# Kernel optimization log

Measured on AMD Instinct MI355X. Metric: run time of the kernel, lower is better.

## Reference

```python
import jax, jax.numpy as jnp
import numpy as np

IN_SHAPE = 4096
H_S = 250        # sender_hidden
H_R = 100        # receiver_hidden
MAX_LEN = 30     # message_shape[0]
VOCAB = 40       # message_shape[1]; EOS = VOCAB-1
OUT_CLS = 512 ** 2  # out_shape[1] ** out_shape[0]


def lstm_cell(x, h, c, W_ih, W_hh, b_ih, b_hh):
    # PyTorch LSTM cell: gate order i, f, g, o
    gates = W_ih @ x + b_ih + W_hh @ h + b_hh
    i, f, g, o = jnp.split(gates, 4)
    c_new = jax.nn.sigmoid(f) * c + jax.nn.sigmoid(i) * jnp.tanh(g)
    h_new = jax.nn.sigmoid(o) * jnp.tanh(c_new)
    return h_new, c_new


def setup_inputs() -> dict:
    key = jax.random.key(0)
    ks = jax.random.split(key, 16)
    s = 0.05
    return {
        "x": jax.random.normal(ks[0], (IN_SHAPE,), dtype=jnp.float32),
        "gumbel_noise": jax.random.gumbel(ks[1], (MAX_LEN, VOCAB), dtype=jnp.float32),
        "W_s1": jax.random.normal(ks[2], (H_S, IN_SHAPE)) * s,
        "b_s1": jnp.zeros((H_S,), jnp.float32),
        "W_ih1": jax.random.normal(ks[3], (4 * H_S, VOCAB)) * s,
        "W_hh1": jax.random.normal(ks[4], (4 * H_S, H_S)) * s,
        "b_ih1": jnp.zeros((4 * H_S,), jnp.float32),
        "b_hh1": jnp.zeros((4 * H_S,), jnp.float32),
        "W_p": jax.random.normal(ks[5], (VOCAB, H_S)) * s,
        "b_p": jnp.zeros((VOCAB,), jnp.float32),
        "W_ih2": jax.random.normal(ks[6], (4 * H_R, VOCAB)) * s,
        "W_hh2": jax.random.normal(ks[7], (4 * H_R, H_R)) * s,
        "b_ih2": jnp.zeros((4 * H_R,), jnp.float32),
        "b_hh2": jnp.zeros((4 * H_R,), jnp.float32),
        "W_r": jax.random.normal(ks[8], (OUT_CLS, H_R)) * s,
        "b_r": jnp.zeros((OUT_CLS,), jnp.float32),
    }


def reference(x, gumbel_noise, W_s1, b_s1, W_ih1, W_hh1, b_ih1, b_hh1,
              W_p, b_p, W_ih2, W_hh2, b_ih2, b_hh2, W_r, b_r):
    dt = x.dtype
    eos = jax.nn.one_hot(VOCAB - 1, VOCAB, dtype=dt)
    # sender: h0 = relu(sender1(x)), c0 = 0, first input = sos = zeros
    h0 = jax.nn.relu(W_s1 @ x + b_s1)
    c0 = jnp.zeros((H_S,), dt)
    sos = jnp.zeros((VOCAB,), dt)
    is_last = jnp.arange(MAX_LEN) == MAX_LEN - 1

    def sender_step(carry, inp):
        h, c, sym, done = carry
        g, last = inp
        nh, nc = lstm_cell(sym, h, c, W_ih1, W_hh1, b_ih1, b_hh1)
        logits = W_p @ nh + b_p
        soft = jax.nn.softmax(logits + g)  # gumbel_softmax, tau=1
        idx = jnp.argmax(soft)
        hard = jax.nn.one_hot(idx, VOCAB, dtype=dt)
        st = hard + soft - jax.lax.stop_gradient(soft)  # straight-through
        # at max length the original appends the plain EOS constant
        emit = jnp.where(last & ~done, eos, st)
        emit = jnp.where(done, eos, emit)
        valid = ~done  # this symbol is part of the message
        new_done = done | (idx == VOCAB - 1) | last
        h = jnp.where(done, h, nh)
        c = jnp.where(done, c, nc)
        sym = jnp.where(done, sym, emit)
        return (h, c, sym, new_done), (emit, valid)

    _, (msg, valid) = jax.lax.scan(
        sender_step, (h0, c0, sos, jnp.array(False)), (gumbel_noise, is_last))

    # receiver LSTM: consume message up to and including first EOS (freeze after)
    def recv_step(carry, inp):
        h, c = carry
        sym, v = inp
        nh, nc = lstm_cell(sym, h, c, W_ih2, W_hh2, b_ih2, b_hh2)
        return (jnp.where(v, nh, h), jnp.where(v, nc, c)), None

    (hR, _), _ = jax.lax.scan(
        recv_step, (jnp.zeros((H_R,), dt), jnp.zeros((H_R,), dt)), (msg, valid))
    return jax.nn.softmax(W_r @ hR + b_r)  # [OUT_CLS]
```

## Files before the change

### kernel.cpp

```cpp
#include <hip/hip_runtime.h>
#include <math.h>

#define HS    250
#define HRr   100
#define VOC   40
#define TMAX  30
#define NCLS  262144
#define KS    10
#define RPB   25

typedef unsigned long long ull;

#define PKNH(wsp, par) ((ull*)(wsp) + (size_t)(par) * 256)
#define PKLP(wsp, par) ((ull*)(wsp) + 512 + (size_t)(par) * 400)
#define PKMSG(wsp)     ((ull*)(wsp) + 1312)
#define WS_SUMS 5024
#define WS_HR   5088
#define WS_ZERO_BYTES 20352

#define TG(wv) ((unsigned)((wv) >> 32))

__device__ __forceinline__ float sigf(float x) { return 1.f / (1.f + expf(-x)); }
__device__ __forceinline__ float lanebc(float v, int l) {
  return __int_as_float(__builtin_amdgcn_readlane(__float_as_int(v), l));
}
__device__ __forceinline__ ull packtv(unsigned tag, float v) {
  return ((ull)tag << 32) | (ull)__float_as_uint(v);
}
__device__ __forceinline__ float lowf(ull w) { return __uint_as_float((unsigned)w); }

__device__ __forceinline__ void st_llc(ull* p, ull v) {
  asm volatile("global_store_dwordx2 %0, %1, off sc0 sc1"
               :: "v"(p), "v"(v) : "memory");
}
__device__ __forceinline__ ull ld_llc(const ull* p) {
  ull r;
  asm volatile("global_load_dwordx2 %0, %1, off sc0 sc1\n\t"
               "s_waitcnt vmcnt(0)"
               : "=v"(r) : "v"(p) : "memory");
  return r;
}

#define SENDER_GATES(P, HV)                                   \
  {                                                           \
    _Pragma("unroll")                                         \
    for (int i = 0; i < 64; i += 4) {                         \
      a0 += whh[i    ] * lanebc(HV, i    );                   \
      a1 += whh[i + 1] * lanebc(HV, i + 1);                   \
      a2 += whh[i + 2] * lanebc(HV, i + 2);                   \
      a3 += whh[i + 3] * lanebc(HV, i + 3);                   \
    }                                                         \
    _Pragma("unroll")                                         \
    for (int i = 0; i < 10; i += 2) {                         \
      a0 += wih[i    ] * lanebc(sv, (P) * 10 + i    );        \
      a1 += wih[i + 1] * lanebc(sv, (P) * 10 + i + 1);        \
    }                                                         \
  }

#define RED(x) ((part[(x)] + part[100 + (x)]) + (part[200 + (x)] + part[300 + (x)]))

__global__ __launch_bounds__(512, 2) void k_sender(
    const float* __restrict__ x,
    const float* __restrict__ W_s1,  const float* __restrict__ b_s1,
    const float* __restrict__ gum,
    const float* __restrict__ W_ih1, const float* __restrict__ W_hh1,
    const float* __restrict__ b_ih1, const float* __restrict__ b_hh1,
    const float* __restrict__ W_p,   const float* __restrict__ b_p,
    const float* __restrict__ W_ih2, const float* __restrict__ W_hh2,
    const float* __restrict__ b_ih2, const float* __restrict__ b_hh2,
    float* __restrict__ ws) {
  __shared__ float part[400];
  __shared__ float h0L[32];
  __shared__ float hx[256];
  __shared__ float lpx[400];
  __shared__ float symx[VOC];
  __shared__ int   doneL;
  __shared__ float gL[400];
  __shared__ float hL[HRr];

  const int b    = blockIdx.x;
  const int t0   = threadIdx.x;
  const int lane = t0 & 63;
  const int w    = t0 >> 6;

  if (b < KS) {
    const int p    = w & 3;
    const int lr   = ((w >> 2) << 6) + lane;
    const bool gact = (lr < 100);
    const int gi   = lr / 25, rr = lr % 25;
    const int grow = gi * 250 + b * RPB + rr;

    float whh[64], wih[10], bsum = 0.f;
    if (gact) {
      #pragma unroll
      for (int i = 0; i < 64; i++) {
        int k = p * 64 + i;
        whh[i] = (k < HS) ? W_hh1[(size_t)grow * HS + k] : 0.f;
      }
      #pragma unroll
      for (int i = 0; i < 10; i++) wih[i] = W_ih1[grow * VOC + p * 10 + i];
      bsum = b_ih1[grow] + b_hh1[grow];
    }
    float wps[RPB];
    if (w == 0) {
      #pragma unroll
      for (int r = 0; r < RPB; r++)
        wps[r] = (lane < VOC) ? W_p[lane * HS + b * RPB + r] : 0.f;
    }
    const float bpv = (lane < VOC) ? b_p[lane] : 0.f;

    {
      const int nr = (w == 7) ? 4 : 3;
      for (int j = 0; j < nr; ++j) {
        const int r = 3 * w + j;
        const float4* wr = (const float4*)(W_s1 + (size_t)(b * RPB + r) * 4096);
        const float4* xr = (const float4*)x;
        float a0 = 0.f, a1 = 0.f, a2 = 0.f, a3 = 0.f;
        #pragma unroll
        for (int q = 0; q < 16; ++q) {
          float4 w4 = wr[lane + (q << 6)], x4 = xr[lane + (q << 6)];
          a0 += w4.x * x4.x; a1 += w4.y * x4.y; a2 += w4.z * x4.z; a3 += w4.w * x4.w;
        }
        float acc = (a0 + a1) + (a2 + a3);
        #pragma unroll
        for (int o = 32; o; o >>= 1) acc += __shfl_down(acc, o);
        if (lane == 0) h0L[r] = acc + b_s1[b * RPB + r];
      }
    }
    __syncthreads();
    if (w == 0 && lane < RPB) {
      float hn0 = fmaxf(h0L[lane], 0.f);
      st_llc(&PKNH(ws, 1)[b * RPB + lane], packtv(1u, hn0));
    }

    float c  = 0.f;
    float sv = 0.f;
    const bool h3v = (192 + lane) < HS;
    const bool l6v = lane < (400 - 384);

    for (int s = 0; s <= TMAX; ++s) {
      float gv = 0.f;
      if (s > 0 && lane < VOC) gv = gum[(s - 1) * VOC + lane];

      if (w == 0) {
        const unsigned need = (unsigned)(s + 1);
        const int par = (s + 1) & 1;
        const ull* nhp = PKNH(ws, par);
        const ull* lpp = PKLP(ws, par);
        const bool lpact = (s > 0);
        const ull* pn0 = nhp + lane;        const ull* pn1 = nhp + 64 + lane;
        const ull* pn2 = nhp + 128 + lane;  const ull* pn3 = nhp + 192 + lane;
        const ull* pl0 = lpp + lane;        const ull* pl1 = lpp + 64 + lane;
        const ull* pl2 = lpp + 128 + lane;  const ull* pl3 = lpp + 192 + lane;
        const ull* pl4 = lpp + 256 + lane;  const ull* pl5 = lpp + 320 + lane;
        const ull* pl6 = lpp + 384 + lane;
        ull hw0, hw1, hw2, hw3, lw0, lw1, lw2, lw3, lw4, lw5, lw6;
        for (;;) {
          asm volatile(
            "global_load_dwordx2 %0, %11, off sc0 sc1\n\t"
            "global_load_dwordx2 %1, %12, off sc0 sc1\n\t"
            "global_load_dwordx2 %2, %13, off sc0 sc1\n\t"
            "global_load_dwordx2 %3, %14, off sc0 sc1\n\t"
            "global_load_dwordx2 %4, %15, off sc0 sc1\n\t"
            "global_load_dwordx2 %5, %16, off sc0 sc1\n\t"
            "global_load_dwordx2 %6, %17, off sc0 sc1\n\t"
            "global_load_dwordx2 %7, %18, off sc0 sc1\n\t"
            "global_load_dwordx2 %8, %19, off sc0 sc1\n\t"
            "global_load_dwordx2 %9, %20, off sc0 sc1\n\t"
            "global_load_dwordx2 %10, %21, off sc0 sc1\n\t"
            "s_waitcnt vmcnt(0)"
            : "=&v"(hw0), "=&v"(hw1), "=&v"(hw2), "=&v"(hw3),
              "=&v"(lw0), "=&v"(lw1), "=&v"(lw2), "=&v"(lw3),
              "=&v"(lw4), "=&v"(lw5), "=&v"(lw6)
            : "v"(pn0), "v"(pn1), "v"(pn2), "v"(pn3),
              "v"(pl0), "v"(pl1), "v"(pl2), "v"(pl3),
              "v"(pl4), "v"(pl5), "v"(pl6)
            : "memory");
          bool ok = TG(hw0) == need && TG(hw1) == need && TG(hw2) == need &&
                    (!h3v || TG(hw3) == need);
          if (lpact) {
            ok = ok && TG(lw0) == need && TG(lw1) == need && TG(lw2) == need &&
                       TG(lw3) == need && TG(lw4) == need && TG(lw5) == need &&
                       (!l6v || TG(lw6) == need);
          }
          if (__all(ok)) break;
        }
        hx[lane] = lowf(hw0); hx[64 + lane] = lowf(hw1); hx[128 + lane] = lowf(hw2);
        if (h3v) hx[192 + lane] = lowf(hw3);
        if (lpact) {
          lpx[lane] = lowf(lw0);        lpx[64 + lane] = lowf(lw1);
          lpx[128 + lane] = lowf(lw2);  lpx[192 + lane] = lowf(lw3);
          lpx[256 + lane] = lowf(lw4);  lpx[320 + lane] = lowf(lw5);
          if (l6v) lpx[384 + lane] = lowf(lw6);
        }
      }
      __syncthreads();

      float hv0 = hx[lane], hv1 = hx[64 + lane], hv2 = hx[128 + lane];
      float hv3 = h3v ? hx[192 + lane] : 0.f;

      if (s > 0) {
        float lg = -INFINITY;
        if (lane < VOC) {
          float acc = bpv + gv;
          #pragma unroll
          for (int m = 0; m < KS; ++m) acc += lpx[m * VOC + lane];
          lg = acc;
        }
        float v = lg; int bi = lane;
        #pragma unroll
        for (int o = 32; o; o >>= 1) {
          float ov = __shfl_down(v, o);
          int   oi = __shfl_down(bi, o);
          if (ov > v) { v = ov; bi = oi; }
        }
        float m  = __shfl(v, 0);
        int  idx = __shfl(bi, 0);
        float e = (lane < VOC) ? expf(lg - m) : 0.f;
        float ssum = e;
        #pragma unroll
        for (int o = 32; o; o >>= 1) ssum += __shfl_down(ssum, o);
        ssum = __shfl(ssum, 0);
        float soft = e / ssum;
        float hard = (lane == idx) ? 1.f : 0.f;
        float st   = (hard + soft) - soft;
        const bool last = (s - 1 == TMAX - 1);
        float emit = last ? ((lane == VOC - 1) ? 1.f : 0.f) : st;
        const bool done = (idx == VOC - 1) || last;
        if (b == 0 && w == 0 && lane < VOC)
          st_llc(&PKMSG(ws)[(s - 1) * VOC + lane],
                 packtv((unsigned)s | (done ? 0x10000u : 0u), emit));
        sv = (lane < VOC) ? emit : 0.f;
        if (done) break;
      }

      if (gact) {
        float a0 = bsum, a1 = 0.f, a2 = 0.f, a3 = 0.f;
        if      (p == 0) SENDER_GATES(0, hv0)
        else if (p == 1) SENDER_GATES(1, hv1)
        else if (p == 2) SENDER_GATES(2, hv2)
        else             SENDER_GATES(3, hv3)
        part[p * 100 + lr] = (a0 + a1) + (a2 + a3);
      }
      __syncthreads();

      if (w == 0) {
        float gi_ = RED(lane < RPB ? lane : 0);
        float gf_ = RED(25 + (lane < RPB ? lane : 0));
        float gg_ = RED(50 + (lane < RPB ? lane : 0));
        float go_ = RED(75 + (lane < RPB ? lane : 0));
        float ig = sigf(gi_), fg = sigf(gf_), gg = tanhf(gg_), og = sigf(go_);
        float cn = fg * c + ig * gg; c = cn;
        float hn = og * tanhf(cn);
        float lpsum = 0.f;
        #pragma unroll
        for (int r = 0; r < RPB; ++r) lpsum += wps[r] * lanebc(hn, r);
        const unsigned nt = (unsigned)(s + 2);
        const int np = (s + 2) & 1;
        if (lane < RPB) st_llc(&PKNH(ws, np)[b * RPB + lane], packtv(nt, hn));
        if (lane < VOC) st_llc(&PKLP(ws, np)[b * VOC + lane], packtv(nt, lpsum));
      }
    }
  } else {
    const bool act = (t0 < 400);
    float wih2[VOC], whh2[HRr], bsum2 = 0.f;
    if (act) {
      #pragma unroll
      for (int i = 0; i < VOC; i++) wih2[i] = W_ih2[t0 * VOC + i];
      #pragma unroll
      for (int i = 0; i < HRr; i++) whh2[i] = W_hh2[t0 * HRr + i];
      bsum2 = b_ih2[t0] + b_hh2[t0];
    }
    float c2 = 0.f, rv0 = 0.f, rv1 = 0.f;

    for (int t = 0; t < TMAX; ++t) {
      if (w == 0) {
        const bool mv = (lane < VOC);
        ull mw = 0;
        for (;;) {
          if (mv) mw = ld_llc(&PKMSG(ws)[t * VOC + lane]);
          bool ok = !mv || ((unsigned)(mw >> 32) & 0xFFFFu) == (unsigned)(t + 1);
          if (__all(ok)) break;
        }
        if (mv) symx[lane] = lowf(mw);
        if (lane == 0) doneL = (int)(((unsigned)(mw >> 32)) >> 16);
      }
      __syncthreads();
      const bool done = (doneL != 0);
      float sv2 = (lane < VOC) ? symx[lane] : 0.f;
      if (act) {
        float a0 = bsum2, a1 = 0.f, a2 = 0.f, a3 = 0.f;
        #pragma unroll
        for (int i = 0; i < VOC; i += 4) {
          a0 += wih2[i    ] * lanebc(sv2, i    );
          a1 += wih2[i + 1] * lanebc(sv2, i + 1);
          a2 += wih2[i + 2] * lanebc(sv2, i + 2);
          a3 += wih2[i + 3] * lanebc(sv2, i + 3);
        }
        #pragma unroll
        for (int i = 0; i < 64; i += 4) {
          a0 += whh2[i    ] * lanebc(rv0, i    );
          a1 += whh2[i + 1] * lanebc(rv0, i + 1);
          a2 += whh2[i + 2] * lanebc(rv0, i + 2);
          a3 += whh2[i + 3] * lanebc(rv0, i + 3);
        }
        #pragma unroll
        for (int i = 0; i < 36; i += 4) {
          a0 += whh2[64 + i    ] * lanebc(rv1, i    );
          a1 += whh2[64 + i + 1] * lanebc(rv1, i + 1);
          a2 += whh2[64 + i + 2] * lanebc(rv1, i + 2);
          a3 += whh2[64 + i + 3] * lanebc(rv1, i + 3);
        }
        gL[t0] = (a0 + a1) + (a2 + a3);
      }
      __syncthreads();
      if (t0 < HRr) {
        float ig = sigf(gL[t0]);
        float fg = sigf(gL[100 + t0]);
        float gg = tanhf(gL[200 + t0]);
        float og = sigf(gL[300 + t0]);
        float cn = fg * c2 + ig * gg; c2 = cn;
        hL[t0] = og * tanhf(cn);
      }
      __syncthreads();
      rv0 = hL[lane];
      rv1 = (lane < 36) ? hL[64 + lane] : 0.f;
      if (done) break;
    }
    if (t0 < HRr) ws[WS_HR + t0] = hL[t0];
  }
}

__global__ __launch_bounds__(256) void k_out(
    const float* __restrict__ W_r, const float* __restrict__ b_r,
    float* __restrict__ ws, float* __restrict__ out) {
  __shared__ float4 h4[25];
  __shared__ float  red[4];
  const int t0 = threadIdx.x;
  if (t0 < 25) h4[t0] = ((const float4*)(ws + WS_HR))[t0];
  __syncthreads();
  const int lane = t0 & 63;
  const int wv   = t0 >> 6;
  const int sl   = lane & 31;
  const int hf   = lane >> 5;
  const int base = blockIdx.x * 128 + wv * 32;
  float accs = 0.f;
  #pragma unroll 4
  for (int i = 0; i < 16; ++i) {
    const int row = base + 2 * i + hf;
    float v = 0.f;
    if (sl < 25) {
      float4 w4 = ((const float4*)W_r)[(size_t)row * 25 + sl];
      float4 hq = h4[sl];
      v = w4.x * hq.x + w4.y * hq.y + w4.z * hq.z + w4.w * hq.w;
    }
    #pragma unroll
    for (int o = 16; o; o >>= 1) v += __shfl_down(v, o, 32);
    float e = 0.f;
    if (sl == 0) { e = expf(v + b_r[row]); accs += e; }
    float eB = __shfl(e, 32);
    if (lane == 0) ((float2*)out)[(base + 2 * i) >> 1] = make_float2(e, eB);
  }
  accs += __shfl_down(accs, 32);
  if (lane == 0) red[wv] = accs;
  __syncthreads();
  if (t0 == 0)
    atomicAdd(&ws[WS_SUMS + (blockIdx.x & 63)], (red[0] + red[1]) + (red[2] + red[3]));
}

__global__ __launch_bounds__(256) void k_scale(const float* __restrict__ ws,
                                               float* __restrict__ out) {
  float s = ws[WS_SUMS + (threadIdx.x & 63)];
  #pragma unroll
  for (int o = 1; o < 64; o <<= 1) s += __shfl_xor(s, o);
  const float rinv = 1.f / s;
  const int i = blockIdx.x * 256 + threadIdx.x;
  float4 e = ((const float4*)out)[i];
  e.x *= rinv; e.y *= rinv; e.z *= rinv; e.w *= rinv;
  ((float4*)out)[i] = e;
}

extern "C" void kernel_launch(void* const* d_in, const int* in_sizes, int n_in,
                              void* d_out, int out_size, void* d_ws, size_t ws_size,
                              hipStream_t stream) {
  const float* x     = (const float*)d_in[0];
  const float* gum   = (const float*)d_in[1];
  const float* W_s1  = (const float*)d_in[2];
  const float* b_s1  = (const float*)d_in[3];
  const float* W_ih1 = (const float*)d_in[4];
  const float* W_hh1 = (const float*)d_in[5];
  const float* b_ih1 = (const float*)d_in[6];
  const float* b_hh1 = (const float*)d_in[7];
  const float* W_p   = (const float*)d_in[8];
  const float* b_p   = (const float*)d_in[9];
  const float* W_ih2 = (const float*)d_in[10];
  const float* W_hh2 = (const float*)d_in[11];
  const float* b_ih2 = (const float*)d_in[12];
  const float* b_hh2 = (const float*)d_in[13];
  const float* W_r   = (const float*)d_in[14];
  const float* b_r   = (const float*)d_in[15];
  float* ws  = (float*)d_ws;
  float* out = (float*)d_out;

  (void)hipMemsetAsync(d_ws, 0, WS_ZERO_BYTES, stream);
  k_sender<<<KS + 1,   512, 0, stream>>>(x, W_s1, b_s1, gum, W_ih1, W_hh1,
                                         b_ih1, b_hh1, W_p, b_p,
                                         W_ih2, W_hh2, b_ih2, b_hh2, ws);
  k_out   <<<NCLS/128, 256, 0, stream>>>(W_r, b_r, ws, out);
  k_scale <<<NCLS/1024,256, 0, stream>>>(ws, out);
}
```

Baseline: 304.3 us.

## Compute sender logits locally from full hidden state instead of exchanging partial sums

Each sender block now computes all 40 logits redundantly from the full gathered hidden vector using W_p rows held in registers (5 rows per wave) with wave reductions. This removes the per-step publication and polling of 400 tagged partial-logit words through the coherent cache, shrinking the cross-block exchange to just the hidden state. It adds redundant compute, an extra block barrier per step and more registers, and the launch bound is relaxed to one block per SM to allow that register growth.

```diff
diff --git a/kernel.cpp b/kernel.cpp
--- a/kernel.cpp
+++ b/kernel.cpp
@@ -12,7 +12,6 @@
 typedef unsigned long long ull;
 
 #define PKNH(wsp, par) ((ull*)(wsp) + (size_t)(par) * 256)
-#define PKLP(wsp, par) ((ull*)(wsp) + 512 + (size_t)(par) * 400)
 #define PKMSG(wsp)     ((ull*)(wsp) + 1312)
 #define WS_SUMS 5024
 #define WS_HR   5088
@@ -59,7 +58,7 @@
 
 #define RED(x) ((part[(x)] + part[100 + (x)]) + (part[200 + (x)] + part[300 + (x)]))
 
-__global__ __launch_bounds__(512, 2) void k_sender(
+__global__ __launch_bounds__(512, 1) void k_sender(
     const float* __restrict__ x,
     const float* __restrict__ W_s1,  const float* __restrict__ b_s1,
     const float* __restrict__ gum,
@@ -72,7 +71,7 @@
   __shared__ float part[400];
   __shared__ float h0L[32];
   __shared__ float hx[256];
-  __shared__ float lpx[400];
+  __shared__ float logitsL[40];
   __shared__ float symx[VOC];
   __shared__ int   doneL;
   __shared__ float gL[400];
@@ -101,11 +100,19 @@
       for (int i = 0; i < 10; i++) wih[i] = W_ih1[grow * VOC + p * 10 + i];
       bsum = b_ih1[grow] + b_hh1[grow];
     }
-    float wps[RPB];
-    if (w == 0) {
-      #pragma unroll
-      for (int r = 0; r < RPB; r++)
-        wps[r] = (lane < VOC) ? W_p[lane * HS + b * RPB + r] : 0.f;
+    const bool h3v = (192 + lane) < HS;
+
+    float wpv[5][4];
+    {
+      const int row0 = 5 * w;
+      #pragma unroll
+      for (int r = 0; r < 5; ++r) {
+        const float* wr = W_p + (size_t)(row0 + r) * HS;
+        wpv[r][0] = wr[lane];
+        wpv[r][1] = wr[64 + lane];
+        wpv[r][2] = wr[128 + lane];
+        wpv[r][3] = h3v ? wr[192 + lane] : 0.f;
+      }
     }
     const float bpv = (lane < VOC) ? b_p[lane] : 0.f;
 
@@ -135,8 +142,6 @@
 
     float c  = 0.f;
     float sv = 0.f;
-    const bool h3v = (192 + lane) < HS;
-    const bool l6v = lane < (400 - 384);
 
     for (int s = 0; s <= TMAX; ++s) {
       float gv = 0.f;
@@ -146,53 +151,25 @@
         const unsigned need = (unsigned)(s + 1);
         const int par = (s + 1) & 1;
         const ull* nhp = PKNH(ws, par);
-        const ull* lpp = PKLP(ws, par);
-        const bool lpact = (s > 0);
         const ull* pn0 = nhp + lane;        const ull* pn1 = nhp + 64 + lane;
         const ull* pn2 = nhp + 128 + lane;  const ull* pn3 = nhp + 192 + lane;
-        const ull* pl0 = lpp + lane;        const ull* pl1 = lpp + 64 + lane;
-        const ull* pl2 = lpp + 128 + lane;  const ull* pl3 = lpp + 192 + lane;
-        const ull* pl4 = lpp + 256 + lane;  const ull* pl5 = lpp + 320 + lane;
-        const ull* pl6 = lpp + 384 + lane;
-        ull hw0, hw1, hw2, hw3, lw0, lw1, lw2, lw3, lw4, lw5, lw6;
+        ull hw0, hw1, hw2, hw3;
         for (;;) {
           asm volatile(
-            "global_load_dwordx2 %0, %11, off sc0 sc1\n\t"
-            "global_load_dwordx2 %1, %12, off sc0 sc1\n\t"
-            "global_load_dwordx2 %2, %13, off sc0 sc1\n\t"
-            "global_load_dwordx2 %3, %14, off sc0 sc1\n\t"
-            "global_load_dwordx2 %4, %15, off sc0 sc1\n\t"
-            "global_load_dwordx2 %5, %16, off sc0 sc1\n\t"
-            "global_load_dwordx2 %6, %17, off sc0 sc1\n\t"
-            "global_load_dwordx2 %7, %18, off sc0 sc1\n\t"
-            "global_load_dwordx2 %8, %19, off sc0 sc1\n\t"
-            "global_load_dwordx2 %9, %20, off sc0 sc1\n\t"
-            "global_load_dwordx2 %10, %21, off sc0 sc1\n\t"
+            "global_load_dwordx2 %0, %4, off sc0 sc1\n\t"
+            "global_load_dwordx2 %1, %5, off sc0 sc1\n\t"
+            "global_load_dwordx2 %2, %6, off sc0 sc1\n\t"
+            "global_load_dwordx2 %3, %7, off sc0 sc1\n\t"
             "s_waitcnt vmcnt(0)"
-            : "=&v"(hw0), "=&v"(hw1), "=&v"(hw2), "=&v"(hw3),
-              "=&v"(lw0), "=&v"(lw1), "=&v"(lw2), "=&v"(lw3),
-              "=&v"(lw4), "=&v"(lw5), "=&v"(lw6)
-            : "v"(pn0), "v"(pn1), "v"(pn2), "v"(pn3),
-              "v"(pl0), "v"(pl1), "v"(pl2), "v"(pl3),
-              "v"(pl4), "v"(pl5), "v"(pl6)
+            : "=&v"(hw0), "=&v"(hw1), "=&v"(hw2), "=&v"(hw3)
+            : "v"(pn0), "v"(pn1), "v"(pn2), "v"(pn3)
             : "memory");
           bool ok = TG(hw0) == need && TG(hw1) == need && TG(hw2) == need &&
                     (!h3v || TG(hw3) == need);
-          if (lpact) {
-            ok = ok && TG(lw0) == need && TG(lw1) == need && TG(lw2) == need &&
-                       TG(lw3) == need && TG(lw4) == need && TG(lw5) == need &&
-                       (!l6v || TG(lw6) == need);
-          }
           if (__all(ok)) break;
         }
         hx[lane] = lowf(hw0); hx[64 + lane] = lowf(hw1); hx[128 + lane] = lowf(hw2);
         if (h3v) hx[192 + lane] = lowf(hw3);
-        if (lpact) {
-          lpx[lane] = lowf(lw0);        lpx[64 + lane] = lowf(lw1);
-          lpx[128 + lane] = lowf(lw2);  lpx[192 + lane] = lowf(lw3);
-          lpx[256 + lane] = lowf(lw4);  lpx[320 + lane] = lowf(lw5);
-          if (l6v) lpx[384 + lane] = lowf(lw6);
-        }
       }
       __syncthreads();
 
@@ -200,13 +177,18 @@
       float hv3 = h3v ? hx[192 + lane] : 0.f;
 
       if (s > 0) {
+        #pragma unroll
+        for (int r = 0; r < 5; ++r) {
+          float pp = (wpv[r][0] * hv0 + wpv[r][1] * hv1) +
+                     (wpv[r][2] * hv2 + wpv[r][3] * hv3);
+          #pragma unroll
+          for (int o = 32; o; o >>= 1) pp += __shfl_down(pp, o);
+          if (lane == 0) logitsL[5 * w + r] = pp;
+        }
+        __syncthreads();
+
         float lg = -INFINITY;
-        if (lane < VOC) {
-          float acc = bpv + gv;
-          #pragma unroll
-          for (int m = 0; m < KS; ++m) acc += lpx[m * VOC + lane];
-          lg = acc;
-        }
+        if (lane < VOC) lg = bpv + gv + logitsL[lane];
         float v = lg; int bi = lane;
         #pragma unroll
         for (int o = 32; o; o >>= 1) {
@@ -252,13 +234,9 @@
         float ig = sigf(gi_), fg = sigf(gf_), gg = tanhf(gg_), og = sigf(go_);
         float cn = fg * c + ig * gg; c = cn;
         float hn = og * tanhf(cn);
-        float lpsum = 0.f;
-        #pragma unroll
-        for (int r = 0; r < RPB; ++r) lpsum += wps[r] * lanebc(hn, r);
         const unsigned nt = (unsigned)(s + 2);
         const int np = (s + 2) & 1;
         if (lane < RPB) st_llc(&PKNH(ws, np)[b * RPB + lane], packtv(nt, hn));
-        if (lane < VOC) st_llc(&PKLP(ws, np)[b * VOC + lane], packtv(nt, lpsum));
       }
     }
   } else {
```

New measurement: 329.1 us. 8.2% more time.
